# Kernel tuning notes

Measured on AMD Instinct MI355X. Metric: run time of the kernel, lower is better.

Reference implementation:

```python
import jax, jax.numpy as jnp
import numpy as np

FEATURES = 1024
DEPTH = int(np.floor(np.log2(FEATURES)))  # 10
NODES = 2 ** DEPTH - 1                    # 1023


def _unit_rows(key, shape):
    w = jax.random.normal(key, shape, dtype=jnp.float32)
    return w / jnp.linalg.norm(w, axis=-1, keepdims=True)


def setup_inputs() -> dict:
    key = jax.random.key(0)
    k_x, k_X, k_Y = jax.random.split(key, 3)
    oldx = jax.random.normal(k_x, (8, 4096, FEATURES), dtype=jnp.float32)
    X = _unit_rows(k_X, (NODES, FEATURES))  # hyperspherical-shell init
    Y = _unit_rows(k_Y, (NODES, FEATURES))
    return {"oldx": oldx, "X": X, "Y": Y}


def reference(oldx, X, Y):
    features = X.shape[-1]
    x = oldx.reshape(-1, features)            # [B, F]
    B = x.shape[0]
    cur = jnp.zeros((B,), dtype=jnp.int32)    # per-sample tree node
    y = jnp.zeros_like(x)
    for _ in range(DEPTH):                    # fixed small depth loop (10)
        Xc = X[cur]                           # [B, F] data-dependent gather
        lam = jnp.einsum('bi,bi->b', x, Xc)   # [B]
        y = y + lam[:, None] * Y[cur]         # [B, F]
        cur = cur * 2 + 1 + (lam > 0).astype(jnp.int32)
    return y.reshape(oldx.shape)
```

## Files before the change

### kernel.cpp

```cpp
#include <hip/hip_runtime.h>

#define FEAT 1024
#define DEPTH 10
#define NLEAF 1024
#define NODES (NLEAF - 1)
#define CAP 320
#define TAU 1e-3f

typedef float f32x4 __attribute__((ext_vector_type(4)));

template <int CTRL, int RMASK>
__device__ __forceinline__ float dpp_shift_f(float v) {
    union { float f; int i; } u, r;
    u.f = v;
    r.i = __builtin_amdgcn_update_dpp(0, u.i, CTRL, RMASK, 0xF, true);
    return r.f;
}

__device__ __forceinline__ float wave_sum_f32(float v) {
    v += dpp_shift_f<0x111, 0xF>(v);
    v += dpp_shift_f<0x112, 0xF>(v);
    v += dpp_shift_f<0x114, 0xF>(v);
    v += dpp_shift_f<0x118, 0xF>(v);
    v += dpp_shift_f<0x142, 0xA>(v);
    v += dpp_shift_f<0x143, 0xC>(v);
    union { float f; int i; } u, r;
    u.f = v;
    r.i = __builtin_amdgcn_readlane(u.i, 63);
    return r.f;
}

template <int CTRL, int RMASK>
__device__ __forceinline__ double dpp_shift_d(double v) {
    union { double d; int i[2]; } u, r;
    u.d = v;
    r.i[0] = __builtin_amdgcn_update_dpp(0, u.i[0], CTRL, RMASK, 0xF, true);
    r.i[1] = __builtin_amdgcn_update_dpp(0, u.i[1], CTRL, RMASK, 0xF, true);
    return r.d;
}

__device__ __forceinline__ double wave_sum_f64(double v) {
    v += dpp_shift_d<0x111, 0xF>(v);
    v += dpp_shift_d<0x112, 0xF>(v);
    v += dpp_shift_d<0x114, 0xF>(v);
    v += dpp_shift_d<0x118, 0xF>(v);
    v += dpp_shift_d<0x142, 0xA>(v);
    v += dpp_shift_d<0x143, 0xC>(v);
    union { double d; int i[2]; } u, r;
    u.d = v;
    r.i[0] = __builtin_amdgcn_readlane(u.i[0], 63);
    r.i[1] = __builtin_amdgcn_readlane(u.i[1], 63);
    return r.d;
}

__device__ __forceinline__ double dot_f64(const f32x4* xv, const f32x4* xc) {
    double p0 = 0.0, p1 = 0.0, p2 = 0.0, p3 = 0.0;
#pragma unroll
    for (int k = 0; k < 4; ++k) {
        p0 += (double)xv[k][0] * (double)xc[k][0];
        p1 += (double)xv[k][1] * (double)xc[k][1];
        p2 += (double)xv[k][2] * (double)xc[k][2];
        p3 += (double)xv[k][3] * (double)xc[k][3];
    }
    return wave_sum_f64((p0 + p1) + (p2 + p3));
}

__global__ __launch_bounds__(1024) void zero_kernel(int* __restrict__ cursor) {
    cursor[threadIdx.x] = 0;
}

__global__ __launch_bounds__(256) void path_kernel(
    const float* __restrict__ x,
    const float* __restrict__ Xw,
    float* __restrict__ lam_out,
    int* __restrict__ order,
    int* __restrict__ cursor,
    int nsamples)
{
    const int wave = threadIdx.x >> 6;
    const int lane = threadIdx.x & 63;
    const int sA = (blockIdx.x * 4 + wave) * 2;
    const int sB = sA + 1;
    if (sA >= nsamples) return;

    const float* xpA = x + (size_t)sA * FEAT;
    const float* xpB = x + (size_t)sB * FEAT;
    f32x4 xvA[4], xvB[4];
#pragma unroll
    for (int k = 0; k < 4; ++k) {
        xvA[k] = __builtin_nontemporal_load(
            reinterpret_cast<const f32x4*>(xpA + (lane + 64 * k) * 4));
        xvB[k] = __builtin_nontemporal_load(
            reinterpret_cast<const f32x4*>(xpB + (lane + 64 * k) * 4));
    }

    int curA = 0, curB = 0;
#pragma unroll
    for (int d = 0; d < DEPTH; ++d) {
        const float* XrA = Xw + (size_t)curA * FEAT;
        const float* XrB = Xw + (size_t)curB * FEAT;

        f32x4 xcA[4], xcB[4];
#pragma unroll
        for (int k = 0; k < 4; ++k) {
            xcA[k] = *reinterpret_cast<const f32x4*>(XrA + (lane + 64 * k) * 4);
            xcB[k] = *reinterpret_cast<const f32x4*>(XrB + (lane + 64 * k) * 4);
        }

        float a0 = 0.f, a1 = 0.f, a2 = 0.f, a3 = 0.f;
        float b0 = 0.f, b1 = 0.f, b2 = 0.f, b3 = 0.f;
#pragma unroll
        for (int k = 0; k < 4; ++k) {
            a0 = fmaf(xvA[k][0], xcA[k][0], a0);
            a1 = fmaf(xvA[k][1], xcA[k][1], a1);
            a2 = fmaf(xvA[k][2], xcA[k][2], a2);
            a3 = fmaf(xvA[k][3], xcA[k][3], a3);
            b0 = fmaf(xvB[k][0], xcB[k][0], b0);
            b1 = fmaf(xvB[k][1], xcB[k][1], b1);
            b2 = fmaf(xvB[k][2], xcB[k][2], b2);
            b3 = fmaf(xvB[k][3], xcB[k][3], b3);
        }
        const float pA32 = wave_sum_f32((a0 + a1) + (a2 + a3));
        const float pB32 = wave_sum_f32((b0 + b1) + (b2 + b3));

        double pA, pB;
        if (__builtin_expect(__builtin_fabsf(pA32) < TAU, 0))
            pA = dot_f64(xvA, xcA);
        else
            pA = (double)pA32;
        if (__builtin_expect(__builtin_fabsf(pB32) < TAU, 0))
            pB = dot_f64(xvB, xcB);
        else
            pB = (double)pB32;

        if (lane == 0) {
            lam_out[(size_t)sA * DEPTH + d] = (float)pA;
            lam_out[(size_t)sB * DEPTH + d] = (float)pB;
        }
        curA = 2 * curA + 1 + (pA > 0.0 ? 1 : 0);
        curB = 2 * curB + 1 + (pB > 0.0 ? 1 : 0);
    }

    if (lane == 0) {
        const int bA = curA - NODES;
        const int bB = curB - NODES;
        const int pA_ = atomicAdd(&cursor[bA], 1);
        const int pB_ = atomicAdd(&cursor[bB], 1);
        if (pA_ < CAP) order[bA * CAP + pA_] = sA;
        if (pB_ < CAP) order[bB * CAP + pB_] = sB;
    }
}

__global__ __launch_bounds__(512) void emit_kernel(
    const float* __restrict__ Yw,
    const float* __restrict__ lam,
    const int* __restrict__ order,
    const int* __restrict__ cursor,
    float* __restrict__ out)
{
    __shared__ float ylds[DEPTH][FEAT];
    const int b = blockIdx.x >> 1;
    const int half = blockIdx.x & 1;
    const int leafPlus = b + NLEAF;

    for (int i = threadIdx.x; i < DEPTH * (FEAT / 4); i += 512) {
        const int d = i >> 8;
        const int c = i & 255;
        const int node = (leafPlus >> (DEPTH - d)) - 1;
        reinterpret_cast<f32x4*>(ylds[d])[c] =
            reinterpret_cast<const f32x4*>(Yw + (size_t)node * FEAT)[c];
    }
    __syncthreads();

    int cnt = cursor[b];
    if (cnt > CAP) cnt = CAP;
    const int wave = threadIdx.x >> 6;
    const int lane = threadIdx.x & 63;

    for (int i = half * 8 + wave; i < cnt; i += 16) {
        const int s = __builtin_amdgcn_readfirstlane(order[b * CAP + i]);

        const float* lp = lam + (size_t)s * DEPTH;
        float lm[DEPTH];
#pragma unroll
        for (int d = 0; d < DEPTH; ++d)
            lm[d] = lp[d];

        float* op = out + (size_t)s * FEAT;
#pragma unroll
        for (int k = 0; k < 4; ++k) {
            f32x4 o = (f32x4)(0.f);
#pragma unroll
            for (int d = 0; d < DEPTH; ++d)
                o += lm[d] * reinterpret_cast<const f32x4*>(ylds[d])[lane + 64 * k];
            __builtin_nontemporal_store(o, reinterpret_cast<f32x4*>(op + 4 * (lane + 64 * k)));
        }
    }
}

__global__ __launch_bounds__(256) void fff_fallback(
    const float* __restrict__ x, const float* __restrict__ Xw,
    const float* __restrict__ Yw, float* __restrict__ out, int nsamples)
{
    const int wave = threadIdx.x >> 6, lane = threadIdx.x & 63;
    const int s = blockIdx.x * 4 + wave;
    if (s >= nsamples) return;
    const float* xp = x + (size_t)s * FEAT;
    f32x4 xv[4], acc[4];
#pragma unroll
    for (int k = 0; k < 4; ++k) {
        xv[k] = *reinterpret_cast<const f32x4*>(xp + (lane + 64 * k) * 4);
        acc[k] = (f32x4)(0.f);
    }
    int cur = 0;
#pragma unroll
    for (int d = 0; d < DEPTH; ++d) {
        const float* Xr = Xw + (size_t)cur * FEAT;
        double p = 0.0;
#pragma unroll
        for (int k = 0; k < 4; ++k) {
            f32x4 xc = *reinterpret_cast<const f32x4*>(Xr + (lane + 64 * k) * 4);
            p += (double)xv[k][0] * (double)xc[0];
            p += (double)xv[k][1] * (double)xc[1];
            p += (double)xv[k][2] * (double)xc[2];
            p += (double)xv[k][3] * (double)xc[3];
        }
#pragma unroll
        for (int off = 32; off >= 1; off >>= 1) p += __shfl_xor(p, off, 64);
        const float lamv = (float)p;
        const float* Yr = Yw + (size_t)cur * FEAT;
#pragma unroll
        for (int k = 0; k < 4; ++k) {
            f32x4 yc = *reinterpret_cast<const f32x4*>(Yr + (lane + 64 * k) * 4);
            acc[k] += lamv * yc;
        }
        cur = 2 * cur + 1 + (p > 0.0 ? 1 : 0);
    }
    float* op = out + (size_t)s * FEAT;
#pragma unroll
    for (int k = 0; k < 4; ++k)
        *reinterpret_cast<f32x4*>(op + 4 * (lane + 64 * k)) = acc[k];
}

extern "C" void kernel_launch(void* const* d_in, const int* in_sizes, int n_in,
                              void* d_out, int out_size, void* d_ws, size_t ws_size,
                              hipStream_t stream) {
    const float* oldx = (const float*)d_in[0];
    const float* Xw   = (const float*)d_in[1];
    const float* Yw   = (const float*)d_in[2];
    float* out = (float*)d_out;

    const int ns = in_sizes[0] / FEAT;

    const size_t lamB  = (size_t)ns * DEPTH * sizeof(float);
    const size_t ordB  = (size_t)NLEAF * CAP * sizeof(int);
    const size_t curB  = NLEAF * sizeof(int);
    const size_t need  = lamB + ordB + curB;

    if (ws_size < need) {
        fff_fallback<<<(ns + 3) / 4, 256, 0, stream>>>(oldx, Xw, Yw, out, ns);
        return;
    }

    char* w = (char*)d_ws;
    float* lam    = (float*)w;  w += lamB;
    int*   order  = (int*)w;    w += ordB;
    int*   cursor = (int*)w;

    zero_kernel<<<1, 1024, 0, stream>>>(cursor);
    path_kernel<<<(ns + 7) / 8, 256, 0, stream>>>(oldx, Xw, lam, order, cursor, ns);
    emit_kernel<<<2 * NLEAF, 512, 0, stream>>>(Yw, lam, order, cursor, out);
}
```

Baseline: 112.5 us.

## Gather bf16 copy of routing weights in path kernel with fp64 fallback

```diff
diff --git a/kernel.cpp b/kernel.cpp
--- a/kernel.cpp
+++ b/kernel.cpp
@@ -5,9 +5,10 @@
 #define NLEAF 1024
 #define NODES (NLEAF - 1)
 #define CAP 320
-#define TAU 1e-3f
+#define TAU 0.02f
 
 typedef float f32x4 __attribute__((ext_vector_type(4)));
+typedef unsigned int uint32_t_;
 
 template <int CTRL, int RMASK>
 __device__ __forceinline__ float dpp_shift_f(float v) {
@@ -53,25 +54,45 @@
     return r.d;
 }
 
-__device__ __forceinline__ double dot_f64(const f32x4* xv, const f32x4* xc) {
+__device__ __attribute__((noinline)) double dot_f64_row(
+    const f32x4* xv, const float* Xr, int lane)
+{
     double p0 = 0.0, p1 = 0.0, p2 = 0.0, p3 = 0.0;
 #pragma unroll
     for (int k = 0; k < 4; ++k) {
-        p0 += (double)xv[k][0] * (double)xc[k][0];
-        p1 += (double)xv[k][1] * (double)xc[k][1];
-        p2 += (double)xv[k][2] * (double)xc[k][2];
-        p3 += (double)xv[k][3] * (double)xc[k][3];
+        f32x4 xc = *reinterpret_cast<const f32x4*>(Xr + (lane + 64 * k) * 4);
+        p0 += (double)xv[k][0] * (double)xc[0];
+        p1 += (double)xv[k][1] * (double)xc[1];
+        p2 += (double)xv[k][2] * (double)xc[2];
+        p3 += (double)xv[k][3] * (double)xc[3];
     }
     return wave_sum_f64((p0 + p1) + (p2 + p3));
 }
 
-__global__ __launch_bounds__(1024) void zero_kernel(int* __restrict__ cursor) {
-    cursor[threadIdx.x] = 0;
+__global__ __launch_bounds__(256) void prep_kernel(
+    const float* __restrict__ Xw,
+    unsigned short* __restrict__ Xb,
+    int* __restrict__ cursor)
+{
+    const int gid = blockIdx.x * 256 + threadIdx.x;
+    const int r = gid >> 10;
+    const int o = gid & 1023;
+    const int lane = o >> 4, j = o & 15;
+    const int src = ((lane + 64 * (j >> 2)) << 2) + (j & 3);
+
+    union { float f; unsigned int u; } v;
+    v.f = Xw[(size_t)r * FEAT + src];
+    unsigned int u = v.u;
+    u += 0x7FFFu + ((u >> 16) & 1u);
+    Xb[(size_t)r * FEAT + o] = (unsigned short)(u >> 16);
+
+    if (gid < NLEAF) cursor[gid] = 0;
 }
 
 __global__ __launch_bounds__(256) void path_kernel(
     const float* __restrict__ x,
     const float* __restrict__ Xw,
+    const unsigned short* __restrict__ Xb,
     float* __restrict__ lam_out,
     int* __restrict__ order,
     int* __restrict__ cursor,
@@ -97,39 +118,46 @@
     int curA = 0, curB = 0;
 #pragma unroll
     for (int d = 0; d < DEPTH; ++d) {
-        const float* XrA = Xw + (size_t)curA * FEAT;
-        const float* XrB = Xw + (size_t)curB * FEAT;
-
-        f32x4 xcA[4], xcB[4];
-#pragma unroll
-        for (int k = 0; k < 4; ++k) {
-            xcA[k] = *reinterpret_cast<const f32x4*>(XrA + (lane + 64 * k) * 4);
-            xcB[k] = *reinterpret_cast<const f32x4*>(XrB + (lane + 64 * k) * 4);
-        }
+        const uint4* brA = reinterpret_cast<const uint4*>(Xb + (size_t)curA * FEAT + lane * 16);
+        const uint4* brB = reinterpret_cast<const uint4*>(Xb + (size_t)curB * FEAT + lane * 16);
+        const uint4 qA0 = brA[0], qA1 = brA[1];
+        const uint4 qB0 = brB[0], qB1 = brB[1];
+
+        const unsigned int uA[8] = {qA0.x, qA0.y, qA0.z, qA0.w, qA1.x, qA1.y, qA1.z, qA1.w};
+        const unsigned int uB[8] = {qB0.x, qB0.y, qB0.z, qB0.w, qB1.x, qB1.y, qB1.z, qB1.w};
 
         float a0 = 0.f, a1 = 0.f, a2 = 0.f, a3 = 0.f;
         float b0 = 0.f, b1 = 0.f, b2 = 0.f, b3 = 0.f;
 #pragma unroll
         for (int k = 0; k < 4; ++k) {
-            a0 = fmaf(xvA[k][0], xcA[k][0], a0);
-            a1 = fmaf(xvA[k][1], xcA[k][1], a1);
-            a2 = fmaf(xvA[k][2], xcA[k][2], a2);
-            a3 = fmaf(xvA[k][3], xcA[k][3], a3);
-            b0 = fmaf(xvB[k][0], xcB[k][0], b0);
-            b1 = fmaf(xvB[k][1], xcB[k][1], b1);
-            b2 = fmaf(xvB[k][2], xcB[k][2], b2);
-            b3 = fmaf(xvB[k][3], xcB[k][3], b3);
+            union { unsigned int u; float f; } c0, c1, c2, c3, e0, e1, e2, e3;
+            c0.u = uA[2 * k] << 16;
+            c1.u = uA[2 * k] & 0xFFFF0000u;
+            c2.u = uA[2 * k + 1] << 16;
+            c3.u = uA[2 * k + 1] & 0xFFFF0000u;
+            a0 = fmaf(xvA[k][0], c0.f, a0);
+            a1 = fmaf(xvA[k][1], c1.f, a1);
+            a2 = fmaf(xvA[k][2], c2.f, a2);
+            a3 = fmaf(xvA[k][3], c3.f, a3);
+            e0.u = uB[2 * k] << 16;
+            e1.u = uB[2 * k] & 0xFFFF0000u;
+            e2.u = uB[2 * k + 1] << 16;
+            e3.u = uB[2 * k + 1] & 0xFFFF0000u;
+            b0 = fmaf(xvB[k][0], e0.f, b0);
+            b1 = fmaf(xvB[k][1], e1.f, b1);
+            b2 = fmaf(xvB[k][2], e2.f, b2);
+            b3 = fmaf(xvB[k][3], e3.f, b3);
         }
         const float pA32 = wave_sum_f32((a0 + a1) + (a2 + a3));
         const float pB32 = wave_sum_f32((b0 + b1) + (b2 + b3));
 
         double pA, pB;
         if (__builtin_expect(__builtin_fabsf(pA32) < TAU, 0))
-            pA = dot_f64(xvA, xcA);
+            pA = dot_f64_row(xvA, Xw + (size_t)curA * FEAT, lane);
         else
             pA = (double)pA32;
         if (__builtin_expect(__builtin_fabsf(pB32) < TAU, 0))
-            pB = dot_f64(xvB, xcB);
+            pB = dot_f64_row(xvB, Xw + (size_t)curB * FEAT, lane);
         else
             pB = (double)pB32;
 
@@ -252,10 +280,11 @@
 
     const int ns = in_sizes[0] / FEAT;
 
+    const size_t XbB   = (size_t)NODES * FEAT * sizeof(unsigned short);
     const size_t lamB  = (size_t)ns * DEPTH * sizeof(float);
     const size_t ordB  = (size_t)NLEAF * CAP * sizeof(int);
     const size_t curB  = NLEAF * sizeof(int);
-    const size_t need  = lamB + ordB + curB;
+    const size_t need  = XbB + lamB + ordB + curB;
 
     if (ws_size < need) {
         fff_fallback<<<(ns + 3) / 4, 256, 0, stream>>>(oldx, Xw, Yw, out, ns);
@@ -263,11 +292,12 @@
     }
 
     char* w = (char*)d_ws;
+    unsigned short* Xb = (unsigned short*)w;  w += XbB;
     float* lam    = (float*)w;  w += lamB;
     int*   order  = (int*)w;    w += ordB;
     int*   cursor = (int*)w;
 
-    zero_kernel<<<1, 1024, 0, stream>>>(cursor);
-    path_kernel<<<(ns + 7) / 8, 256, 0, stream>>>(oldx, Xw, lam, order, cursor, ns);
+    prep_kernel<<<(NODES * FEAT) / 256, 256, 0, stream>>>(Xw, Xb, cursor);
+    path_kernel<<<(ns + 7) / 8, 256, 0, stream>>>(oldx, Xw, Xb, lam, order, cursor, ns);
     emit_kernel<<<2 * NLEAF, 512, 0, stream>>>(Yw, lam, order, cursor, out);
 }
```

Result: slower. 133.5 us (+18.6%).
